# Optimization experiments

Measured on AMD Instinct MI355X. Metric: run time of the kernel, lower is better.

Reference implementation:

```python
import jax, jax.numpy as jnp
import numpy as np

N = 100000   # nodes
E = 1600000  # edges (before self-loops)
D = 128      # in_feats
H = 128      # n_hidden


def setup_inputs() -> dict:
    key = jax.random.key(0)
    k = jax.random.split(key, 6)
    x = jax.random.normal(k[0], (N, D), dtype=jnp.float32)
    src = jax.random.randint(k[1], (E,), 0, N, dtype=jnp.int32)
    dst = jax.random.randint(k[2], (E,), 0, N, dtype=jnp.int32)
    W1 = jax.random.normal(k[3], (D, H), dtype=jnp.float32) / np.float32(np.sqrt(D))
    b1 = jnp.zeros((H,), jnp.float32)
    W2 = jax.random.normal(k[4], (H, H), dtype=jnp.float32) / np.float32(np.sqrt(H))
    b2 = jnp.zeros((H,), jnp.float32)
    return {"x": x, "src": src, "dst": dst, "W1": W1, "b1": b1, "W2": W2, "b2": b2}


def _gcn(x, src, dst, W1, b1, W2, b2):
    n = x.shape[0]
    # add_self_loop(g)
    loops = jnp.arange(n, dtype=src.dtype)
    s = jnp.concatenate([src, loops])
    d = jnp.concatenate([dst, loops])
    ones = jnp.ones((s.shape[0],), dtype=x.dtype)
    deg_out = jax.ops.segment_sum(ones, s, num_segments=n)  # src out-degree
    deg_in = jax.ops.segment_sum(ones, d, num_segments=n)   # dst in-degree
    # DGL GraphConv norm='both': D_out^{-1/2} on source side, D_in^{-1/2} on dest side
    norm_out = jax.lax.rsqrt(jnp.maximum(deg_out, 1.0))[:, None]
    norm_in = jax.lax.rsqrt(jnp.maximum(deg_in, 1.0))[:, None]

    def layer(h, W, b):
        h = h * norm_out                                   # [n, f]
        agg = jax.ops.segment_sum(h[s], d, num_segments=n)  # gather + scatter-add over edges
        return (agg * norm_in) @ W + b

    h = layer(x, W1, b1)
    # dropout p=0 -> identity
    h = layer(h, W2, b2)
    return h


def reference(x, src, dst, W1, b1, W2, b2):
    return _gcn(x, src, dst, W1, b1, W2, b2)
```

## Files before the change

### kernel.cpp

```cpp
#include <hip/hip_runtime.h>

#define FD 128
#define SHIFT 10
#define BNODES 1024
#define NBK 128
#define CHUNK 8192
#define ST 512
#define NIT 16

typedef unsigned int u32;
typedef unsigned short u16;
typedef unsigned char u8;
typedef __attribute__((ext_vector_type(8))) short short8;
typedef __attribute__((ext_vector_type(4))) float f32x4;
typedef __attribute__((ext_vector_type(4))) u32 u32x4;

__device__ inline u16 f2bf(float f) {
  u32 u = __float_as_uint(f);
  u += 0x7fffu + ((u >> 16) & 1u);
  return (u16)(u >> 16);
}
__device__ inline float bf2f(u16 h) { return __uint_as_float((u32)h << 16); }

__global__ __launch_bounds__(512) void k_histpw(
    const int* __restrict__ src, const int* __restrict__ dst,
    int* __restrict__ bcntD, int* __restrict__ bcntS, int e, int n, int nbuck,
    const float* __restrict__ W1, u32* __restrict__ wf1hi, u32* __restrict__ wf1lo,
    const float* __restrict__ W2, u32* __restrict__ wf2hi, u32* __restrict__ wf2lo) {
  int tid = threadIdx.x;
  if (blockIdx.x >= 256) {
    int gi = (blockIdx.x - 256) * 512 + tid;
    int i = gi & 8191;
    const float* W = (gi < 8192) ? W1 : W2;
    u32* wfhi = (gi < 8192) ? wf1hi : wf2hi;
    u32* wflo = (gi < 8192) ? wf1lo : wf2lo;
    int m = i & 3, l = (i >> 2) & 63, f = i >> 8;
    int kt = f & 3, nt = f >> 2;
    int k0 = kt * 32 + ((l >> 4) << 3) + 2 * m;
    int c = nt * 16 + (l & 15);
    float w0 = W[k0 * FD + c], w1 = W[(k0 + 1) * FD + c];
    u16 h0 = f2bf(w0), h1 = f2bf(w1);
    u16 l0 = f2bf(w0 - bf2f(h0)), l1 = f2bf(w1 - bf2f(h1));
    wfhi[i] = (u32)h0 | ((u32)h1 << 16);
    wflo[i] = (u32)l0 | ((u32)l1 << 16);
    return;
  }
  __shared__ int shD[NBK];
  __shared__ int shS[NBK];
  if (tid < NBK) { shD[tid] = 0; shS[tid] = 0; }
  __syncthreads();
  int total = e + n;
  for (int t = blockIdx.x * 512 + tid; t < total; t += 256 * 512) {
    if (t < e) {
      atomicAdd(&shD[dst[t] >> SHIFT], 1);
      atomicAdd(&shS[src[t] >> SHIFT], 1);
    } else {
      atomicAdd(&shD[(t - e) >> SHIFT], 1);
    }
  }
  __syncthreads();
  if (tid < nbuck) {
    if (shD[tid]) atomicAdd(&bcntD[tid], shD[tid]);
    if (shS[tid]) atomicAdd(&bcntS[tid], shS[tid]);
  }
}

__global__ __launch_bounds__(NBK) void k_bscan(
    const int* __restrict__ bcntD, const int* __restrict__ bcntS,
    int* __restrict__ bbaseD, int* __restrict__ bcurD,
    int* __restrict__ bbaseS, int* __restrict__ bcurS,
    int nbuck, int totalD, int totalS) {
  __shared__ int shD[NBK];
  __shared__ int shS[NBK];
  int tid = threadIdx.x;
  int vD = (tid < nbuck) ? bcntD[tid] : 0;
  int vS = (tid < nbuck) ? bcntS[tid] : 0;
  shD[tid] = vD; shS[tid] = vS;
  __syncthreads();
  for (int off = 1; off < NBK; off <<= 1) {
    int aD = (tid >= off) ? shD[tid - off] : 0;
    int aS = (tid >= off) ? shS[tid - off] : 0;
    __syncthreads();
    shD[tid] += aD; shS[tid] += aS;
    __syncthreads();
  }
  if (tid < nbuck) {
    int exD = shD[tid] - vD; bbaseD[tid] = exD; bcurD[tid] = exD;
    int exS = shS[tid] - vS; bbaseS[tid] = exS; bcurS[tid] = exS;
  }
  if (tid == 0) { bbaseD[nbuck] = totalD; bbaseS[nbuck] = totalS; }
}

__global__ __launch_bounds__(ST) void k_scatgx(
    const int* __restrict__ src, const int* __restrict__ dst,
    int* __restrict__ bcurD, int* __restrict__ bcurS,
    u32* __restrict__ pairs, u16* __restrict__ pairs2,
    int e, int n, int nbuck, int nsc,
    const float* __restrict__ x,
    const u32* __restrict__ wfhi, const u32* __restrict__ wflo,
    u32* __restrict__ tout) {
  __shared__ __align__(16) u8 smem[45056];
  int tid512 = threadIdx.x;

  if (blockIdx.x >= (unsigned)nsc) {
    int u = tid512 >> 8, tid = tid512 & 255;
    u32* Au = (u32*)smem + u * 4096;
    int lane = tid & 63;
    int mt = tid >> 6;
    int r0 = ((blockIdx.x - nsc) * 2 + u) * 64;

    #pragma unroll
    for (int it = 0; it < 16; ++it) {
      int w = it * 256 + tid;
      int row = w >> 6, uu = w & 63;
      int grow = r0 + row;
      float2 v = make_float2(0.f, 0.f);
      if (grow < n) v = *(const float2*)(x + (size_t)grow * FD + uu * 2);
      Au[row * 64 + (uu ^ ((row & 7) << 2))] = (u32)f2bf(v.x) | ((u32)f2bf(v.y) << 16);
    }
    __syncthreads();

    short8 afh[4];
    int arow = mt * 16 + (lane & 15);
    #pragma unroll
    for (int kt = 0; kt < 4; ++kt) {
      int boff = arow * 256 + ((kt * 64 + (lane >> 4) * 16) ^ ((arow & 7) << 4));
      afh[kt] = *(const short8*)((const char*)Au + boff);
    }
    __syncthreads();

    for (int nt = 0; nt < 8; ++nt) {
      f32x4 oacc = {0.f, 0.f, 0.f, 0.f};
      #pragma unroll
      for (int kt = 0; kt < 4; ++kt) {
        int f = nt * 4 + kt;
        short8 wh = *(const short8*)(wfhi + (size_t)(f * 64 + lane) * 4);
        short8 wl = *(const short8*)(wflo + (size_t)(f * 64 + lane) * 4);
        oacc = __builtin_amdgcn_mfma_f32_16x16x32_bf16(afh[kt], wh, oacc, 0, 0, 0);
        oacc = __builtin_amdgcn_mfma_f32_16x16x32_bf16(afh[kt], wl, oacc, 0, 0, 0);
      }
      int c = nt * 16 + (lane & 15);
      #pragma unroll
      for (int j = 0; j < 4; ++j) {
        int lrow = mt * 16 + (lane >> 4) * 4 + j;
        ((u16*)Au)[lrow * 128 + c] = f2bf(oacc[j]);
      }
    }
    __syncthreads();
    #pragma unroll
    for (int it = 0; it < 4; ++it) {
      int ci = it * 256 + tid;
      int lrow = ci >> 4, chk = ci & 15;
      int row = r0 + lrow;
      if (row < n)
        *(u32x4*)(tout + (size_t)row * 64 + chk * 4) =
            *(const u32x4*)(Au + lrow * 64 + chk * 4);
    }
    return;
  }

  int* histD = (int*)smem;
  int* exclD = histD + NBK;
  int* gbaseD = exclD + NBK;
  int* rankD = gbaseD + NBK;
  int* histS = rankD + NBK;
  int* exclS = histS + NBK;
  int* gbaseS = exclS + NBK;
  int* rankS = gbaseS + NBK;
  u32* stgv = (u32*)(smem + 4096);
  u8*  stgb = smem + 36864;
  u16* stg2 = (u16*)(smem + 4096);
  u8*  stg2b = smem + 20480;
  int tid = tid512;
  int c0 = blockIdx.x * CHUNK;
  int total = e + n;
  if (tid < NBK) { histD[tid] = 0; histS[tid] = 0; }
  __syncthreads();
  u32 pv_[NIT]; int bD_[NIT], bS_[NIT]; bool v_[NIT], vs_[NIT];
  #pragma unroll
  for (int i = 0; i < NIT; ++i) {
    int t = c0 + i * ST + tid;
    v_[i] = (t < total);
    vs_[i] = (t < e);
    pv_[i] = 0; bD_[i] = 0; bS_[i] = 0;
    if (v_[i]) {
      int s, d;
      if (vs_[i]) { s = src[t]; d = dst[t]; }
      else        { s = t - e;  d = s; }
      pv_[i] = ((u32)(d & (BNODES - 1)) << 22) | (u32)s;
      bD_[i] = d >> SHIFT;
      atomicAdd(&histD[bD_[i]], 1);
      if (vs_[i]) { bS_[i] = s >> SHIFT; atomicAdd(&histS[bS_[i]], 1); }
    }
  }
  __syncthreads();
  int hD = 0, hS = 0;
  if (tid < NBK) { hD = histD[tid]; hS = histS[tid]; }
  __syncthreads();
  for (int off = 1; off < NBK; off <<= 1) {
    int aD = 0, aS = 0;
    if (tid < NBK && tid >= off) { aD = histD[tid - off]; aS = histS[tid - off]; }
    __syncthreads();
    if (tid < NBK) { histD[tid] += aD; histS[tid] += aS; }
    __syncthreads();
  }
  if (tid < NBK) {
    int exD = histD[tid] - hD; exclD[tid] = exD; rankD[tid] = exD;
    int exS = histS[tid] - hS; exclS[tid] = exS; rankS[tid] = exS;
    gbaseD[tid] = (tid < nbuck && hD > 0) ? atomicAdd(&bcurD[tid], hD) : 0;
    gbaseS[tid] = (tid < nbuck && hS > 0) ? atomicAdd(&bcurS[tid], hS) : 0;
  }
  __syncthreads();
  #pragma unroll
  for (int i = 0; i < NIT; ++i) {
    if (v_[i]) {
      int p = atomicAdd(&rankD[bD_[i]], 1);
      stgv[p] = pv_[i];
      stgb[p] = (u8)bD_[i];
    }
  }
  __syncthreads();
  int V = min(CHUNK, total - c0);
  for (int j = tid; j < V; j += ST) {
    int b = stgb[j];
    pairs[gbaseD[b] + (j - exclD[b])] = stgv[j];
  }
  __syncthreads();
  #pragma unroll
  for (int i = 0; i < NIT; ++i) {
    if (vs_[i]) {
      int p = atomicAdd(&rankS[bS_[i]], 1);
      stg2[p] = (u16)(pv_[i] & (BNODES - 1));
      stg2b[p] = (u8)bS_[i];
    }
  }
  __syncthreads();
  int V2 = min(CHUNK, e - c0);
  for (int j = tid; j < V2; j += ST) {
    int b = stg2b[j];
    pairs2[gbaseS[b] + (j - exclS[b])] = stg2[j];
  }
}

__global__ __launch_bounds__(1024) void k_build(
    const u32* __restrict__ pairs, const int* __restrict__ bbase,
    const u16* __restrict__ pairs2, const int* __restrict__ bbaseS,
    int* __restrict__ rp, int* __restrict__ col,
    float* __restrict__ nin, float* __restrict__ nout,
    int n, int nbuck, int total) {
  __shared__ int cnt[BNODES];
  __shared__ int cur[BNODES];
  __shared__ int wsum[16];
  int tid = threadIdx.x;
  if (blockIdx.x >= (unsigned)nbuck) {
    int b = blockIdx.x - nbuck;
    int base = bbaseS[b], end = bbaseS[b + 1];
    cnt[tid] = 0;
    if (b == 0 && tid == 0) nout[n] = 0.f;
    __syncthreads();
    for (int t = base + tid; t < end; t += 1024)
      atomicAdd(&cnt[(int)pairs2[t]], 1);
    __syncthreads();
    int node = (b << SHIFT) + tid;
    if (node < n) nout[node] = rsqrtf((float)(cnt[tid] + 1));
    return;
  }
  int b = blockIdx.x;
  int base = bbase[b], end = bbase[b + 1];
  int node0 = b << SHIFT;
  cnt[tid] = 0;
  __syncthreads();
  for (int t = base + tid; t < end; t += 1024)
    atomicAdd(&cnt[(int)(pairs[t] >> 22)], 1);
  __syncthreads();
  int c = cnt[tid];
  int lane = tid & 63, wv = tid >> 6;
  int v = c;
  #pragma unroll
  for (int o = 1; o < 64; o <<= 1) {
    int t = __shfl_up(v, o, 64);
    if (lane >= o) v += t;
  }
  if (lane == 63) wsum[wv] = v;
  __syncthreads();
  if (tid < 16) {
    int w = wsum[tid];
    #pragma unroll
    for (int o = 1; o < 16; o <<= 1) {
      int t = __shfl_up(w, o, 64);
      if (lane >= o) w += t;
    }
    wsum[tid] = w;
  }
  __syncthreads();
  int incl = v + (wv ? wsum[wv - 1] : 0);
  int ex = incl - c;
  int node = node0 + tid;
  if (node < n) {
    rp[node] = base + ex;
    nin[node] = rsqrtf((float)c);
  }
  if (b == nbuck - 1 && tid == 0) rp[n] = total;
  cur[tid] = ex;
  __syncthreads();
  for (int t = base + tid; t < end; t += 1024) {
    u32 pr = pairs[t];
    int p = atomicAdd(&cur[(int)(pr >> 22)], 1);
    col[base + p] = (int)(pr & 0x3FFFFFu);
  }
}

template <int MODE>
__global__ __launch_bounds__(256) void k_agg(
    const u32* __restrict__ hs, const int* __restrict__ rp,
    const int* __restrict__ col, const float* __restrict__ nin,
    const float* __restrict__ snorm, const float* __restrict__ bias,
    float* __restrict__ fout, u32* __restrict__ hsout, int n) {
  int wid = (blockIdx.x * 256 + threadIdx.x) >> 6;
  int lane = threadIdx.x & 63;
  int g = lane >> 4, ch = lane & 15;
  int r = wid * 4 + g;
  bool valid = (r < n);
  int e0 = 0, e1 = 0;
  if (valid) { e0 = rp[r]; e1 = rp[r + 1]; }
  int m = e1 - e0;
  m = max(m, __shfl_xor(m, 16, 64));
  m = max(m, __shfl_xor(m, 32, 64));
  int trips = (m + 7) >> 3;
  float acc[8] = {0.f, 0.f, 0.f, 0.f, 0.f, 0.f, 0.f, 0.f};
  const u32x4* hv = (const u32x4*)hs;
  int em1 = (e1 > 0) ? (e1 - 1) : 0;
  for (int it = 0; it < trips; ++it) {
    int tb = e0 + it * 8;
    u32x4 buf[8];
    float wb[8];
    #pragma unroll
    for (int u = 0; u < 8; ++u) {
      int idx = tb + u;
      int s = col[min(idx, em1)];
      s = (idx < e1) ? s : n;
      buf[u] = hv[(size_t)s * 16 + ch];
      if (MODE) wb[u] = snorm[s];
    }
    if (MODE) {
      #pragma unroll
      for (int u = 0; u < 8; ++u)
        #pragma unroll
        for (int j = 0; j < 4; ++j) {
          u32 x = buf[u][j];
          acc[2 * j]     = fmaf(__uint_as_float(x << 16), wb[u], acc[2 * j]);
          acc[2 * j + 1] = fmaf(__uint_as_float(x & 0xFFFF0000u), wb[u], acc[2 * j + 1]);
        }
    } else {
      #pragma unroll
      for (int u = 0; u < 8; ++u)
        #pragma unroll
        for (int j = 0; j < 4; ++j) {
          u32 x = buf[u][j];
          acc[2 * j]     += __uint_as_float(x << 16);
          acc[2 * j + 1] += __uint_as_float(x & 0xFFFF0000u);
        }
    }
  }
  if (!valid) return;
  float wi = nin[r];
  float4 b0 = *(const float4*)(bias + ch * 8);
  float4 b1v = *(const float4*)(bias + ch * 8 + 4);
  float v[8];
  v[0] = acc[0] * wi + b0.x;  v[1] = acc[1] * wi + b0.y;
  v[2] = acc[2] * wi + b0.z;  v[3] = acc[3] * wi + b0.w;
  v[4] = acc[4] * wi + b1v.x; v[5] = acc[5] * wi + b1v.y;
  v[6] = acc[6] * wi + b1v.z; v[7] = acc[7] * wi + b1v.w;
  if (MODE == 0) {
    *(float4*)(fout + (size_t)r * FD + ch * 8)     = make_float4(v[0], v[1], v[2], v[3]);
    *(float4*)(fout + (size_t)r * FD + ch * 8 + 4) = make_float4(v[4], v[5], v[6], v[7]);
  } else {
    u32 hi[4];
    #pragma unroll
    for (int j = 0; j < 4; ++j)
      hi[j] = (u32)f2bf(v[2 * j]) | ((u32)f2bf(v[2 * j + 1]) << 16);
    int sch = ch ^ (r & 7);
    u32x4 hq = {hi[0], hi[1], hi[2], hi[3]};
    *(u32x4*)(hsout + (size_t)r * 64 + sch * 4) = hq;
  }
}

__global__ __launch_bounds__(256) void k_gemm2(
    const u32* __restrict__ ahi,
    const u32* __restrict__ wfhi, const u32* __restrict__ wflo,
    const float* __restrict__ nout, u32* __restrict__ yout, int n) {
  __shared__ u32 As[4096];
  int tid = threadIdx.x;
  int lane = tid & 63;
  int mt = tid >> 6;
  int r0 = blockIdx.x * 64;

  const u32x4* gh = (const u32x4*)(ahi + (size_t)r0 * 64);
  u32x4* sh_ = (u32x4*)As;
  #pragma unroll
  for (int t = 0; t < 4; ++t) sh_[t * 256 + tid] = gh[t * 256 + tid];
  __syncthreads();

  short8 afh[4];
  int arow = mt * 16 + (lane & 15);
  #pragma unroll
  for (int kt = 0; kt < 4; ++kt) {
    int boff = arow * 256 + ((kt * 64 + (lane >> 4) * 16) ^ ((arow & 7) << 4));
    afh[kt] = *(const short8*)((const char*)As + boff);
  }
  __syncthreads();

  float wout[4];
  #pragma unroll
  for (int j = 0; j < 4; ++j) {
    int row = r0 + mt * 16 + (lane >> 4) * 4 + j;
    wout[j] = (row < n) ? nout[row] : 0.f;
  }

  for (int nt = 0; nt < 8; ++nt) {
    f32x4 oacc = {0.f, 0.f, 0.f, 0.f};
    #pragma unroll
    for (int kt = 0; kt < 4; ++kt) {
      int f = nt * 4 + kt;
      short8 wh = *(const short8*)(wfhi + (size_t)(f * 64 + lane) * 4);
      short8 wl = *(const short8*)(wflo + (size_t)(f * 64 + lane) * 4);
      oacc = __builtin_amdgcn_mfma_f32_16x16x32_bf16(afh[kt], wh, oacc, 0, 0, 0);
      oacc = __builtin_amdgcn_mfma_f32_16x16x32_bf16(afh[kt], wl, oacc, 0, 0, 0);
    }
    int c = nt * 16 + (lane & 15);
    #pragma unroll
    for (int j = 0; j < 4; ++j) {
      int lrow = mt * 16 + (lane >> 4) * 4 + j;
      ((u16*)As)[lrow * 128 + c] = f2bf(oacc[j] * wout[j]);
    }
  }
  __syncthreads();
  #pragma unroll
  for (int it = 0; it < 4; ++it) {
    int ci = it * 256 + tid;
    int lrow = ci >> 4, chk = ci & 15;
    int row = r0 + lrow;
    if (row < n)
      *(u32x4*)(yout + (size_t)row * 64 + chk * 4) =
          *(const u32x4*)(As + lrow * 64 + chk * 4);
  }
}

extern "C" void kernel_launch(void* const* d_in, const int* in_sizes, int n_in,
                              void* d_out, int out_size, void* d_ws, size_t ws_size,
                              hipStream_t stream) {
  const float* x  = (const float*)d_in[0];
  const int* src  = (const int*)d_in[1];
  const int* dst  = (const int*)d_in[2];
  const float* W1 = (const float*)d_in[3];
  const float* b1 = (const float*)d_in[4];
  const float* W2 = (const float*)d_in[5];
  const float* b2 = (const float*)d_in[6];
  float* out = (float*)d_out;

  int n = in_sizes[0] / FD;
  int e = in_sizes[1];
  int total = e + n;
  int nbuck = (n + BNODES - 1) >> SHIFT;

  char* ws = (char*)d_ws;
  size_t off = 0;
  auto alloc = [&](size_t bytes) -> void* {
    void* p = ws + off;
    off += (bytes + 255) / 256 * 256;
    return p;
  };
  u32* bufA  = (u32*)alloc((size_t)(n + 16) * 64 * 4);
  u32* t1bf  = bufA;
  u32* y2    = bufA;
  u32* pairs = (u32*)alloc((size_t)total * 4 + 256);
  u32* bufC  = (u32*)alloc((size_t)(n + 64) * 64 * 4);
  u16* pairs2 = (u16*)bufC;
  u32* h1bf  = bufC;
  int* col   = (int*)alloc((size_t)total * 4 + 256);
  int* rp    = (int*)alloc((size_t)(n + 1) * 4);
  float* nin  = (float*)alloc((size_t)n * 4);
  float* nout = (float*)alloc((size_t)(n + 16) * 4);
  int* bcntD  = (int*)alloc(NBK * 4);
  int* bcntS  = (int*)alloc(NBK * 4);
  int* bbaseD = (int*)alloc((NBK + 1) * 4);
  int* bbaseS = (int*)alloc((NBK + 1) * 4);
  int* bcurD  = (int*)alloc(NBK * 4);
  int* bcurS  = (int*)alloc(NBK * 4);
  u32* wf1hi  = (u32*)alloc(8192 * 4);
  u32* wf1lo  = (u32*)alloc(8192 * 4);
  u32* wf2hi  = (u32*)alloc(8192 * 4);
  u32* wf2lo  = (u32*)alloc(8192 * 4);

  hipMemsetAsync(bcntD, 0, (size_t)NBK * 4 * 2, stream);
  hipMemsetAsync(bufA + (size_t)n * 64, 0, 64 * 4, stream);

  k_histpw<<<288, 512, 0, stream>>>(src, dst, bcntD, bcntS, e, n, nbuck,
                                    W1, wf1hi, wf1lo, W2, wf2hi, wf2lo);
  k_bscan<<<1, NBK, 0, stream>>>(bcntD, bcntS, bbaseD, bcurD, bbaseS, bcurS,
                                 nbuck, total, e);
  int nsc = (total + CHUNK - 1) / CHUNK;
  int ngx = (n + 127) / 128;
  k_scatgx<<<nsc + ngx, ST, 0, stream>>>(src, dst, bcurD, bcurS, pairs, pairs2,
                                         e, n, nbuck, nsc, x, wf1hi, wf1lo, t1bf);
  k_build<<<2 * nbuck, 1024, 0, stream>>>(pairs, bbaseD, pairs2, bbaseS,
                                          rp, col, nin, nout, n, nbuck, total);

  int agrid = (n + 15) / 16;
  int ggrid = (n + 63) / 64;
  k_agg<1><<<agrid, 256, 0, stream>>>(t1bf, rp, col, nin, nout, b1,
                                      nullptr, h1bf, n);
  k_gemm2<<<ggrid, 256, 0, stream>>>(h1bf, wf2hi, wf2lo, nout, y2, n);
  k_agg<0><<<agrid, 256, 0, stream>>>(y2, rp, col, nin, nullptr, b2,
                                      out, nullptr, n);
}
```

Baseline: 222.7 us.

## Replace global bucket histogram pass with per-chunk offsets in scatter kernel

New measurement: 217.5 us. -2.3%, faster.

```diff
diff --git a/kernel.cpp b/kernel.cpp
--- a/kernel.cpp
+++ b/kernel.cpp
@@ -22,84 +22,34 @@
 }
 __device__ inline float bf2f(u16 h) { return __uint_as_float((u32)h << 16); }
 
-__global__ __launch_bounds__(512) void k_histpw(
-    const int* __restrict__ src, const int* __restrict__ dst,
-    int* __restrict__ bcntD, int* __restrict__ bcntS, int e, int n, int nbuck,
+__global__ __launch_bounds__(512) void k_prepw(
     const float* __restrict__ W1, u32* __restrict__ wf1hi, u32* __restrict__ wf1lo,
     const float* __restrict__ W2, u32* __restrict__ wf2hi, u32* __restrict__ wf2lo) {
-  int tid = threadIdx.x;
-  if (blockIdx.x >= 256) {
-    int gi = (blockIdx.x - 256) * 512 + tid;
-    int i = gi & 8191;
-    const float* W = (gi < 8192) ? W1 : W2;
-    u32* wfhi = (gi < 8192) ? wf1hi : wf2hi;
-    u32* wflo = (gi < 8192) ? wf1lo : wf2lo;
-    int m = i & 3, l = (i >> 2) & 63, f = i >> 8;
-    int kt = f & 3, nt = f >> 2;
-    int k0 = kt * 32 + ((l >> 4) << 3) + 2 * m;
-    int c = nt * 16 + (l & 15);
-    float w0 = W[k0 * FD + c], w1 = W[(k0 + 1) * FD + c];
-    u16 h0 = f2bf(w0), h1 = f2bf(w1);
-    u16 l0 = f2bf(w0 - bf2f(h0)), l1 = f2bf(w1 - bf2f(h1));
-    wfhi[i] = (u32)h0 | ((u32)h1 << 16);
-    wflo[i] = (u32)l0 | ((u32)l1 << 16);
-    return;
-  }
-  __shared__ int shD[NBK];
-  __shared__ int shS[NBK];
-  if (tid < NBK) { shD[tid] = 0; shS[tid] = 0; }
-  __syncthreads();
-  int total = e + n;
-  for (int t = blockIdx.x * 512 + tid; t < total; t += 256 * 512) {
-    if (t < e) {
-      atomicAdd(&shD[dst[t] >> SHIFT], 1);
-      atomicAdd(&shS[src[t] >> SHIFT], 1);
-    } else {
-      atomicAdd(&shD[(t - e) >> SHIFT], 1);
-    }
-  }
-  __syncthreads();
-  if (tid < nbuck) {
-    if (shD[tid]) atomicAdd(&bcntD[tid], shD[tid]);
-    if (shS[tid]) atomicAdd(&bcntS[tid], shS[tid]);
-  }
-}
-
-__global__ __launch_bounds__(NBK) void k_bscan(
-    const int* __restrict__ bcntD, const int* __restrict__ bcntS,
-    int* __restrict__ bbaseD, int* __restrict__ bcurD,
-    int* __restrict__ bbaseS, int* __restrict__ bcurS,
-    int nbuck, int totalD, int totalS) {
-  __shared__ int shD[NBK];
-  __shared__ int shS[NBK];
-  int tid = threadIdx.x;
-  int vD = (tid < nbuck) ? bcntD[tid] : 0;
-  int vS = (tid < nbuck) ? bcntS[tid] : 0;
-  shD[tid] = vD; shS[tid] = vS;
-  __syncthreads();
-  for (int off = 1; off < NBK; off <<= 1) {
-    int aD = (tid >= off) ? shD[tid - off] : 0;
-    int aS = (tid >= off) ? shS[tid - off] : 0;
-    __syncthreads();
-    shD[tid] += aD; shS[tid] += aS;
-    __syncthreads();
-  }
-  if (tid < nbuck) {
-    int exD = shD[tid] - vD; bbaseD[tid] = exD; bcurD[tid] = exD;
-    int exS = shS[tid] - vS; bbaseS[tid] = exS; bcurS[tid] = exS;
-  }
-  if (tid == 0) { bbaseD[nbuck] = totalD; bbaseS[nbuck] = totalS; }
+  int gi = blockIdx.x * 512 + threadIdx.x;
+  int i = gi & 8191;
+  const float* W = (gi < 8192) ? W1 : W2;
+  u32* whi = (gi < 8192) ? wf1hi : wf2hi;
+  u32* wlo = (gi < 8192) ? wf1lo : wf2lo;
+  int m = i & 3, l = (i >> 2) & 63, f = i >> 8;
+  int kt = f & 3, nt = f >> 2;
+  int k0 = kt * 32 + ((l >> 4) << 3) + 2 * m;
+  int c = nt * 16 + (l & 15);
+  float w0 = W[k0 * FD + c], w1 = W[(k0 + 1) * FD + c];
+  u16 h0 = f2bf(w0), h1 = f2bf(w1);
+  u16 l0 = f2bf(w0 - bf2f(h0)), l1 = f2bf(w1 - bf2f(h1));
+  whi[i] = (u32)h0 | ((u32)h1 << 16);
+  wlo[i] = (u32)l0 | ((u32)l1 << 16);
 }
 
 __global__ __launch_bounds__(ST) void k_scatgx(
     const int* __restrict__ src, const int* __restrict__ dst,
-    int* __restrict__ bcurD, int* __restrict__ bcurS,
     u32* __restrict__ pairs, u16* __restrict__ pairs2,
+    int* __restrict__ ofsD, int* __restrict__ ofsS,
     int e, int n, int nbuck, int nsc,
     const float* __restrict__ x,
     const u32* __restrict__ wfhi, const u32* __restrict__ wflo,
     u32* __restrict__ tout) {
-  __shared__ __align__(16) u8 smem[45056];
+  __shared__ __align__(16) u8 smem[36864];
   int tid512 = threadIdx.x;
 
   if (blockIdx.x >= (unsigned)nsc) {
@@ -160,19 +110,14 @@
   }
 
   int* histD = (int*)smem;
-  int* exclD = histD + NBK;
-  int* gbaseD = exclD + NBK;
-  int* rankD = gbaseD + NBK;
+  int* rankD = histD + NBK;
   int* histS = rankD + NBK;
-  int* exclS = histS + NBK;
-  int* gbaseS = exclS + NBK;
-  int* rankS = gbaseS + NBK;
+  int* rankS = histS + NBK;
   u32* stgv = (u32*)(smem + 4096);
-  u8*  stgb = smem + 36864;
   u16* stg2 = (u16*)(smem + 4096);
-  u8*  stg2b = smem + 20480;
   int tid = tid512;
-  int c0 = blockIdx.x * CHUNK;
+  int blk = blockIdx.x;
+  int c0 = blk * CHUNK;
   int total = e + n;
   if (tid < NBK) { histD[tid] = 0; histS[tid] = 0; }
   __syncthreads();
@@ -205,10 +150,12 @@
     __syncthreads();
   }
   if (tid < NBK) {
-    int exD = histD[tid] - hD; exclD[tid] = exD; rankD[tid] = exD;
-    int exS = histS[tid] - hS; exclS[tid] = exS; rankS[tid] = exS;
-    gbaseD[tid] = (tid < nbuck && hD > 0) ? atomicAdd(&bcurD[tid], hD) : 0;
-    gbaseS[tid] = (tid < nbuck && hS > 0) ? atomicAdd(&bcurS[tid], hS) : 0;
+    int exD = histD[tid] - hD;
+    int exS = histS[tid] - hS;
+    rankD[tid] = exD;
+    rankS[tid] = exS;
+    ofsD[tid * nsc + blk] = exD;
+    ofsS[tid * nsc + blk] = exS;
   }
   __syncthreads();
   #pragma unroll
@@ -216,65 +163,76 @@
     if (v_[i]) {
       int p = atomicAdd(&rankD[bD_[i]], 1);
       stgv[p] = pv_[i];
-      stgb[p] = (u8)bD_[i];
     }
   }
   __syncthreads();
   int V = min(CHUNK, total - c0);
-  for (int j = tid; j < V; j += ST) {
-    int b = stgb[j];
-    pairs[gbaseD[b] + (j - exclD[b])] = stgv[j];
-  }
+  for (int j = tid; j < V; j += ST)
+    pairs[(size_t)blk * CHUNK + j] = stgv[j];
   __syncthreads();
   #pragma unroll
   for (int i = 0; i < NIT; ++i) {
     if (vs_[i]) {
       int p = atomicAdd(&rankS[bS_[i]], 1);
       stg2[p] = (u16)(pv_[i] & (BNODES - 1));
-      stg2b[p] = (u8)bS_[i];
     }
   }
   __syncthreads();
   int V2 = min(CHUNK, e - c0);
-  for (int j = tid; j < V2; j += ST) {
-    int b = stg2b[j];
-    pairs2[gbaseS[b] + (j - exclS[b])] = stg2[j];
-  }
+  for (int j = tid; j < V2; j += ST)
+    pairs2[(size_t)blk * CHUNK + j] = stg2[j];
 }
 
 __global__ __launch_bounds__(1024) void k_build(
-    const u32* __restrict__ pairs, const int* __restrict__ bbase,
-    const u16* __restrict__ pairs2, const int* __restrict__ bbaseS,
+    const u32* __restrict__ pairs, const u16* __restrict__ pairs2,
+    const int* __restrict__ ofsD, const int* __restrict__ ofsS,
     int* __restrict__ rp, int* __restrict__ col,
     float* __restrict__ nin, float* __restrict__ nout,
-    int n, int nbuck, int total) {
+    int n, int nbuck, int nsc, int total) {
   __shared__ int cnt[BNODES];
   __shared__ int cur[BNODES];
   __shared__ int wsum[16];
+  __shared__ int segs[256], sege[256];
   int tid = threadIdx.x;
+  int lane = tid & 63, wv = tid >> 6;
+
   if (blockIdx.x >= (unsigned)nbuck) {
     int b = blockIdx.x - nbuck;
-    int base = bbaseS[b], end = bbaseS[b + 1];
     cnt[tid] = 0;
+    if (tid < nsc) {
+      segs[tid] = tid * CHUNK + ofsS[b * nsc + tid];
+      sege[tid] = tid * CHUNK + ofsS[(b + 1) * nsc + tid];
+    }
     if (b == 0 && tid == 0) nout[n] = 0.f;
     __syncthreads();
-    for (int t = base + tid; t < end; t += 1024)
-      atomicAdd(&cnt[(int)pairs2[t]], 1);
+    for (int sg = wv; sg < nsc; sg += 16)
+      for (int t = segs[sg] + lane; t < sege[sg]; t += 64)
+        atomicAdd(&cnt[(int)pairs2[t]], 1);
     __syncthreads();
     int node = (b << SHIFT) + tid;
     if (node < n) nout[node] = rsqrtf((float)(cnt[tid] + 1));
     return;
   }
+
   int b = blockIdx.x;
-  int base = bbase[b], end = bbase[b + 1];
   int node0 = b << SHIFT;
+  __shared__ int baseSh;
   cnt[tid] = 0;
-  __syncthreads();
-  for (int t = base + tid; t < end; t += 1024)
-    atomicAdd(&cnt[(int)(pairs[t] >> 22)], 1);
-  __syncthreads();
+  if (tid == 0) baseSh = 0;
+  int rowv = 0;
+  if (tid < nsc) {
+    rowv = ofsD[b * nsc + tid];
+    segs[tid] = tid * CHUNK + rowv;
+    sege[tid] = tid * CHUNK + ofsD[(b + 1) * nsc + tid];
+  }
+  __syncthreads();
+  if (tid < nsc && rowv) atomicAdd(&baseSh, rowv);
+  for (int sg = wv; sg < nsc; sg += 16)
+    for (int t = segs[sg] + lane; t < sege[sg]; t += 64)
+      atomicAdd(&cnt[(int)(pairs[t] >> 22)], 1);
+  __syncthreads();
+  int base = baseSh;
   int c = cnt[tid];
-  int lane = tid & 63, wv = tid >> 6;
   int v = c;
   #pragma unroll
   for (int o = 1; o < 64; o <<= 1) {
@@ -303,11 +261,12 @@
   if (b == nbuck - 1 && tid == 0) rp[n] = total;
   cur[tid] = ex;
   __syncthreads();
-  for (int t = base + tid; t < end; t += 1024) {
-    u32 pr = pairs[t];
-    int p = atomicAdd(&cur[(int)(pr >> 22)], 1);
-    col[base + p] = (int)(pr & 0x3FFFFFu);
-  }
+  for (int sg = wv; sg < nsc; sg += 16)
+    for (int t = segs[sg] + lane; t < sege[sg]; t += 64) {
+      u32 pr = pairs[t];
+      int p = atomicAdd(&cur[(int)(pr >> 22)], 1);
+      col[base + p] = (int)(pr & 0x3FFFFFu);
+    }
 }
 
 template <int MODE>
@@ -462,6 +421,8 @@
   int e = in_sizes[1];
   int total = e + n;
   int nbuck = (n + BNODES - 1) >> SHIFT;
+  int nsc = (total + CHUNK - 1) / CHUNK;
+  int ngx = (n + 127) / 128;
 
   char* ws = (char*)d_ws;
   size_t off = 0;
@@ -473,7 +434,7 @@
   u32* bufA  = (u32*)alloc((size_t)(n + 16) * 64 * 4);
   u32* t1bf  = bufA;
   u32* y2    = bufA;
-  u32* pairs = (u32*)alloc((size_t)total * 4 + 256);
+  u32* pairs = (u32*)alloc((size_t)nsc * CHUNK * 4);
   u32* bufC  = (u32*)alloc((size_t)(n + 64) * 64 * 4);
   u16* pairs2 = (u16*)bufC;
   u32* h1bf  = bufC;
@@ -481,30 +442,21 @@
   int* rp    = (int*)alloc((size_t)(n + 1) * 4);
   float* nin  = (float*)alloc((size_t)n * 4);
   float* nout = (float*)alloc((size_t)(n + 16) * 4);
-  int* bcntD  = (int*)alloc(NBK * 4);
-  int* bcntS  = (int*)alloc(NBK * 4);
-  int* bbaseD = (int*)alloc((NBK + 1) * 4);
-  int* bbaseS = (int*)alloc((NBK + 1) * 4);
-  int* bcurD  = (int*)alloc(NBK * 4);
-  int* bcurS  = (int*)alloc(NBK * 4);
+  int* ofsD  = (int*)alloc((size_t)NBK * nsc * 4);
+  int* ofsS  = (int*)alloc((size_t)NBK * nsc * 4);
   u32* wf1hi  = (u32*)alloc(8192 * 4);
   u32* wf1lo  = (u32*)alloc(8192 * 4);
   u32* wf2hi  = (u32*)alloc(8192 * 4);
   u32* wf2lo  = (u32*)alloc(8192 * 4);
 
-  hipMemsetAsync(bcntD, 0, (size_t)NBK * 4 * 2, stream);
   hipMemsetAsync(bufA + (size_t)n * 64, 0, 64 * 4, stream);
 
-  k_histpw<<<288, 512, 0, stream>>>(src, dst, bcntD, bcntS, e, n, nbuck,
-                                    W1, wf1hi, wf1lo, W2, wf2hi, wf2lo);
-  k_bscan<<<1, NBK, 0, stream>>>(bcntD, bcntS, bbaseD, bcurD, bbaseS, bcurS,
-                                 nbuck, total, e);
-  int nsc = (total + CHUNK - 1) / CHUNK;
-  int ngx = (n + 127) / 128;
-  k_scatgx<<<nsc + ngx, ST, 0, stream>>>(src, dst, bcurD, bcurS, pairs, pairs2,
-                                         e, n, nbuck, nsc, x, wf1hi, wf1lo, t1bf);
-  k_build<<<2 * nbuck, 1024, 0, stream>>>(pairs, bbaseD, pairs2, bbaseS,
-                                          rp, col, nin, nout, n, nbuck, total);
+  k_prepw<<<32, 512, 0, stream>>>(W1, wf1hi, wf1lo, W2, wf2hi, wf2lo);
+  k_scatgx<<<nsc + ngx, ST, 0, stream>>>(
+      src, dst, pairs, pairs2, ofsD, ofsS, e, n, nbuck, nsc,
+      x, wf1hi, wf1lo, t1bf);
+  k_build<<<2 * nbuck, 1024, 0, stream>>>(pairs, pairs2, ofsD, ofsS,
+                                          rp, col, nin, nout, n, nbuck, nsc, total);
 
   int agrid = (n + 15) / 16;
   int ggrid = (n + 63) / 64;
```
